# Kernel tuning notes

Hardware: AMD Instinct MI355X
Metric: run time of the kernel (lower is better)

The kernel has to match this reference:

```python
import jax, jax.numpy as jnp
import numpy as np

E = 2048        # embedding_dim
H = 16          # num_q_heads
G = 4           # group_size
HKV = H // G    # num_kv_heads = 4
D = E // H      # q_head_dim = 128
KVD = E // G    # kv_head_dim = 512
B, N = 2, 2048


def setup_inputs() -> dict:
    key = jax.random.key(0)
    ks = jax.random.split(key, 5)
    s = 0.02
    return {
        "x": jax.random.normal(ks[0], (B, N, E), jnp.float32),
        "Wq": jax.random.normal(ks[1], (E, E), jnp.float32) * s,
        "Wk": jax.random.normal(ks[2], (KVD, E), jnp.float32) * s,
        "Wv": jax.random.normal(ks[3], (KVD, E), jnp.float32) * s,
        "Wo": jax.random.normal(ks[4], (E, E), jnp.float32) * s,
    }


def reference(x, Wq, Wk, Wv, Wo):
    b, n, _ = x.shape
    # projections (nn.Linear: y = x @ W.T)
    q = x @ Wq.T                              # (b, n, E)
    k = x @ Wk.T                              # (b, n, KVD)
    v = x @ Wv.T                              # (b, n, KVD)
    # split heads: q -> b h n d with h=H, then (h g) -> g,h layout
    q = q.reshape(b, n, H, D).transpose(0, 2, 1, 3)          # b H n d
    q = q.reshape(b, HKV, G, n, D).transpose(0, 2, 1, 3, 4)  # b g h n d  (h=HKV)
    k = k.reshape(b, n, HKV, D).transpose(0, 2, 1, 3)        # b h s d
    v = v.reshape(b, n, HKV, D).transpose(0, 2, 1, 3)        # b h s d
    scale = 1.0 / jnp.sqrt(jnp.asarray(D, x.dtype))
    scores = jnp.einsum('bghnd,bhsd->bghns', q, k) * scale   # full score tensor
    scores = jax.nn.softmax(scores, axis=-1)
    # dropout p=0.0 -> identity
    o = jnp.einsum('bghns,bhsd->bghnd', scores, v)           # b g h n d
    # rearrange 'b g h n d -> b n (h g) d' then concat heads
    o = o.transpose(0, 3, 2, 1, 4).reshape(b, n, E)          # b n (h g) d -> b n E
    return o @ Wo.T
```

## Files before the change

kernel.cpp:

```cpp
#include <hip/hip_runtime.h>
#include <hip/hip_bf16.h>
#include <cstdint>
#include <cstddef>

using u16 = unsigned short;
typedef __bf16 bf16x8 __attribute__((ext_vector_type(8)));
typedef float f32x4 __attribute__((ext_vector_type(4)));
typedef float f32x16 __attribute__((ext_vector_type(16)));
typedef u16 u16x4 __attribute__((ext_vector_type(4)));
typedef u16 u16x8 __attribute__((ext_vector_type(8)));
typedef uint32_t u32x4 __attribute__((ext_vector_type(4)));

__device__ __forceinline__ u16 f2bf(float f) {
  uint32_t u = __builtin_bit_cast(uint32_t, f);
  u += 0x7FFFu + ((u >> 16) & 1u);
  return (u16)(u >> 16);
}

__device__ __forceinline__ void gld_lds16(const void* g, void* l) {
  __builtin_amdgcn_global_load_lds(
      (const __attribute__((address_space(1))) unsigned int*)g,
      (__attribute__((address_space(3))) unsigned int*)l, 16, 0, 0);
}

#define MFMA16(a, b, c) __builtin_amdgcn_mfma_f32_16x16x32_bf16((a), (b), (c), 0, 0, 0)
#define MFMA32(a, b, c) __builtin_amdgcn_mfma_f32_32x32x16_bf16((a), (b), (c), 0, 0, 0)

__device__ __forceinline__ uint32_t pkbf(float a, float b) {
  uint32_t d;
  asm("v_cvt_pk_bf16_f32 %0, %1, %2" : "=v"(d) : "v"(a), "v"(b));
  return d;
}
__device__ __forceinline__ void swap32(uint32_t& a, uint32_t& b) {
  asm volatile("v_permlane32_swap_b32 %0, %1" : "+v"(a), "+v"(b));
}

__global__ void cvt_kernel(const float* __restrict__ in, u16* __restrict__ out, int n4) {
  int i = blockIdx.x * blockDim.x + threadIdx.x;
  int stride = gridDim.x * blockDim.x;
  for (; i < n4; i += stride) {
    float4 v = reinterpret_cast<const float4*>(in)[i];
    u16x4 o;
    o[0] = f2bf(v.x); o[1] = f2bf(v.y); o[2] = f2bf(v.z); o[3] = f2bf(v.w);
    reinterpret_cast<u16x4*>(out)[i] = o;
  }
}

__global__ void cvt4_kernel(const float* __restrict__ x, const float* __restrict__ Wq,
                            const float* __restrict__ Wk, const float* __restrict__ Wv,
                            u16* __restrict__ xb, u16* __restrict__ Wc) {
  int i = blockIdx.x * blockDim.x + threadIdx.x;
  int stride = gridDim.x * blockDim.x;
  for (; i < 3670016; i += stride) {
    const float* src; u16* dst; int off;
    if (i < 2097152)      { src = x;  dst = xb;            off = i; }
    else if (i < 3145728) { src = Wq; dst = Wc;            off = i - 2097152; }
    else if (i < 3407872) { src = Wk; dst = Wc + 4194304;  off = i - 3145728; }
    else                  { src = Wv; dst = Wc + 5242880;  off = i - 3407872; }
    float4 v = reinterpret_cast<const float4*>(src)[off];
    u16x4 o;
    o[0] = f2bf(v.x); o[1] = f2bf(v.y); o[2] = f2bf(v.z); o[3] = f2bf(v.w);
    reinterpret_cast<u16x4*>(dst)[off] = o;
  }
}

template <bool OUT_BF16>
__global__ __launch_bounds__(256) void gemm_bt(const u16* __restrict__ A,
                                               const u16* __restrict__ B,
                                               void* __restrict__ Cv,
                                               int M, int N, int K) {
  __shared__ __align__(16) u16 Ash[3][128 * 32];
  __shared__ __align__(16) u16 Bsh[3][128 * 32];
  const int tid = threadIdx.x;
  const int w = tid >> 6, lane = tid & 63, ql = lane & 15, g = lane >> 4;
  const int wr = w >> 1, wc = w & 1;
  const int bid = blockIdx.y * gridDim.x + blockIdx.x;
  const int nwg = gridDim.x * gridDim.y;
  const int wg = (bid & 7) * (nwg >> 3) + (bid >> 3);
  const int m0 = (wg / gridDim.x) * 128, n0 = (wg % gridDim.x) * 128;
  const int srow = w * 16 + (lane >> 2);
  const int sk = (lane & 3) * 8;
  const u16* Abase = A + (size_t)(m0 + srow) * K + sk;
  const u16* Bbase = B + (size_t)(n0 + srow) * K + sk;

  f32x4 acc[4][4];
#pragma unroll
  for (int i = 0; i < 4; i++)
#pragma unroll
    for (int j = 0; j < 4; j++) acc[i][j] = f32x4{0.f, 0.f, 0.f, 0.f};

  auto stage = [&](int bi, int tile) {
    const int kt = tile * 32;
    gld_lds16(Abase + kt,                  &Ash[bi][w * 512]);
    gld_lds16(Abase + (size_t)64 * K + kt, &Ash[bi][2048 + w * 512]);
    gld_lds16(Bbase + kt,                  &Bsh[bi][w * 512]);
    gld_lds16(Bbase + (size_t)64 * K + kt, &Bsh[bi][2048 + w * 512]);
  };

  const int nt = K >> 5;
  stage(0, 0);
  stage(1, 1);
  asm volatile("s_waitcnt vmcnt(4)" ::: "memory");
  __builtin_amdgcn_sched_barrier(0);
  __builtin_amdgcn_s_barrier();
  __builtin_amdgcn_sched_barrier(0);

  int cur = 0;
  for (int t = 0; t < nt; ++t) {
    if (t + 2 < nt) {
      int stg = cur + 2; if (stg >= 3) stg -= 3;
      stage(stg, t + 2);
    }
    bf16x8 af[4], bfr[4];
#pragma unroll
    for (int i = 0; i < 4; i++)
      af[i] = *reinterpret_cast<const bf16x8*>(&Ash[cur][(wr * 64 + i * 16 + ql) * 32 + g * 8]);
#pragma unroll
    for (int j = 0; j < 4; j++)
      bfr[j] = *reinterpret_cast<const bf16x8*>(&Bsh[cur][(wc * 64 + j * 16 + ql) * 32 + g * 8]);
    __builtin_amdgcn_s_setprio(1);
#pragma unroll
    for (int i = 0; i < 4; i++)
#pragma unroll
      for (int j = 0; j < 4; j++)
        acc[i][j] = MFMA16(af[i], bfr[j], acc[i][j]);
    __builtin_amdgcn_s_setprio(0);
    if (t + 1 < nt) {
      if (t + 2 < nt) {
        asm volatile("s_waitcnt vmcnt(4)" ::: "memory");
      } else {
        asm volatile("s_waitcnt vmcnt(0)" ::: "memory");
      }
      __builtin_amdgcn_sched_barrier(0);
      __builtin_amdgcn_s_barrier();
      __builtin_amdgcn_sched_barrier(0);
    }
    cur = (cur == 2) ? 0 : cur + 1;
  }

#pragma unroll
  for (int i = 0; i < 4; i++)
#pragma unroll
    for (int j = 0; j < 4; j++)
#pragma unroll
      for (int r = 0; r < 4; r++) {
        const int row = m0 + wr * 64 + i * 16 + g * 4 + r;
        const int col = n0 + wc * 64 + j * 16 + ql;
        if constexpr (OUT_BF16)
          ((u16*)Cv)[(size_t)row * N + col] = f2bf(acc[i][j][r]);
        else
          ((float*)Cv)[(size_t)row * N + col] = acc[i][j][r];
      }
}

__global__ __launch_bounds__(256, 2) void attn_kernel(const u16* __restrict__ QKV,
                                                      u16* __restrict__ O) {
  __shared__ __align__(16) u16 Kb[2][64 * 128];
  __shared__ __align__(16) u16 Vb[3][2][128 * 32];
  const int tid = threadIdx.x, w = tid >> 6, lane = tid & 63;
  const int lq = lane & 31, hi = lane >> 5;
  const int bid = blockIdx.x;
  const int swz = (bid & 7) * 64 + (bid >> 3);
  const int qt = swz & 15;
  const int bh = swz >> 4;
  const int b = bh >> 4, h = bh & 15, hkv = h >> 2;
  const size_t rowb = (size_t)b * 2048;
  const int qbase = qt * 128 + w * 32;

  const u16* Kg = QKV + 2048 + hkv * 128;
  const u16* Vg = QKV + 2560 + hkv * 128;

  bf16x8 bq[8];
  {
    const u16* qp = QKV + (rowb + qbase + lq) * 3072 + h * 128 + hi * 8;
#pragma unroll
    for (int s5 = 0; s5 < 8; s5++)
      bq[s5] = *reinterpret_cast<const bf16x8*>(qp + s5 * 16);
  }

  const int dg = tid & 7, sl = tid >> 3;

  f32x16 oacc[4], lacc;
#pragma unroll
  for (int dt = 0; dt < 4; dt++)
#pragma unroll
    for (int i = 0; i < 16; i++) oacc[dt][i] = 0.f;
#pragma unroll
  for (int i = 0; i < 16; i++) lacc[i] = 0.f;
  float m = -INFINITY;
  const float CEXP = 0.08838834764831845f * 1.4426950408889634f;

  const bf16x8 ones = __builtin_bit_cast(bf16x8,
      u32x4{0x3F803F80u, 0x3F803F80u, 0x3F803F80u, 0x3F803F80u});

  auto stageK = [&](int pb2, int sbase) {
#pragma unroll
    for (int p = 0; p < 4; p++) {
      const int L = p * 2048 + tid * 8;
      const int s = L >> 7;
      const int gI = (L >> 3) & 15;
      gld_lds16(Kg + (rowb + sbase + s) * 3072 + ((gI ^ (s & 7)) << 3),
                &Kb[pb2][p * 2048 + w * 512]);
    }
  };
  auto writeV = [&](int vb3, const u16x8& a00, const u16x8& a01,
                    const u16x8& a10, const u16x8& a11) {
#pragma unroll
    for (int sh2 = 0; sh2 < 2; sh2++)
#pragma unroll
      for (int hf = 0; hf < 2; hf++) {
        const u16x8 v = sh2 ? (hf ? a11 : a10) : (hf ? a01 : a00);
#pragma unroll
        for (int j = 0; j < 8; j++) {
          const int d = dg * 16 + hf * 8 + j;
          const int key = ((d >> 1) ^ (d >> 4)) & 3;
          Vb[vb3][sh2][d * 32 + (sl ^ (key << 3))] = v[j];
        }
      }
  };

#define KFRAG(PB, SH, S5) \
  (*reinterpret_cast<const bf16x8*>(&Kb[PB][((SH)*32 + lq) * 128 + ((((S5)*2 + hi) ^ (lq & 7)) << 3)]))
#define VFRAG(VB, DT, SS) \
  (*reinterpret_cast<const bf16x8*>(&Vb[VB][(SS) >> 1][((DT)*32 + lq) * 32 + \
      ((((SS) & 1) * 16 + hi * 8) ^ (((((DT)*32 + lq) >> 1) ^ (((DT)*32 + lq) >> 4)) & 3) << 3)]))

  u16x8 v00, v01, v10, v11;
  {
    const u16* vp = Vg + (rowb + sl) * 3072 + dg * 16;
    v00 = *reinterpret_cast<const u16x8*>(vp);
    v01 = *reinterpret_cast<const u16x8*>(vp + 8);
    const u16* vp2 = vp + (size_t)32 * 3072;
    v10 = *reinterpret_cast<const u16x8*>(vp2);
    v11 = *reinterpret_cast<const u16x8*>(vp2 + 8);
  }
  stageK(0, 0);
  writeV(0, v00, v01, v10, v11);
  __syncthreads();

  bf16x8 pf0, pf1, pf2, pf3;
  int vprev = 2, vcur = 0, vnext = 1;

#pragma unroll 1
  for (int sb = 0; sb < 32; sb++) {
    const int pb = sb & 1;
    if (sb < 31) {
      const u16* vp = Vg + (rowb + (sb + 1) * 64 + sl) * 3072 + dg * 16;
      v00 = *reinterpret_cast<const u16x8*>(vp);
      v01 = *reinterpret_cast<const u16x8*>(vp + 8);
      const u16* vp2 = vp + (size_t)32 * 3072;
      v10 = *reinterpret_cast<const u16x8*>(vp2);
      v11 = *reinterpret_cast<const u16x8*>(vp2 + 8);
      stageK(pb ^ 1, (sb + 1) * 64);
    }

    f32x16 sc0, sc1;
#pragma unroll
    for (int i = 0; i < 16; i++) { sc0[i] = 0.f; sc1[i] = 0.f; }
    __builtin_amdgcn_s_setprio(1);
#pragma unroll
    for (int s5 = 0; s5 < 8; s5++) {
      sc0 = MFMA32(KFRAG(pb, 0, s5), bq[s5], sc0);
      sc1 = MFMA32(KFRAG(pb, 1, s5), bq[s5], sc1);
    }
    __builtin_amdgcn_s_setprio(0);

    if (sb) {
      __builtin_amdgcn_s_setprio(1);
#pragma unroll
      for (int dt = 0; dt < 4; dt++) {
        oacc[dt] = MFMA32(VFRAG(vprev, dt, 0), pf0, oacc[dt]);
        oacc[dt] = MFMA32(VFRAG(vprev, dt, 1), pf1, oacc[dt]);
        oacc[dt] = MFMA32(VFRAG(vprev, dt, 2), pf2, oacc[dt]);
        oacc[dt] = MFMA32(VFRAG(vprev, dt, 3), pf3, oacc[dt]);
      }
      __builtin_amdgcn_s_setprio(0);
    }

    float u[16];
#pragma unroll
    for (int i = 0; i < 16; i++) u[i] = fmaxf(sc0[i], sc1[i]);
#pragma unroll
    for (int i = 0; i < 8; i++) u[i] = fmaxf(u[i], u[i + 8]);
#pragma unroll
    for (int i = 0; i < 4; i++) u[i] = fmaxf(u[i], u[i + 4]);
    float mx = fmaxf(fmaxf(u[0], u[1]), fmaxf(u[2], u[3]));
    mx = fmaxf(mx, __shfl_xor(mx, 32));

    if (__any((mx - m) * CEXP > 8.0f)) {
      const float mn = fmaxf(m, mx);
      const float corr = exp2f((m - mn) * CEXP);
#pragma unroll
      for (int i = 0; i < 16; i++) lacc[i] *= corr;
#pragma unroll
      for (int dt = 0; dt < 4; dt++)
#pragma unroll
        for (int i = 0; i < 16; i++) oacc[dt][i] *= corr;
      m = mn;
    }

    const float mC = m * CEXP;
    float e0[16], e1[16];
#pragma unroll
    for (int i = 0; i < 16; i++) {
      e0[i] = exp2f(fmaf(sc0[i], CEXP, -mC));
      e1[i] = exp2f(fmaf(sc1[i], CEXP, -mC));
    }
    {
      uint32_t a, bw;
      u32x4 f;
      a = pkbf(e0[0], e0[1]);  bw = pkbf(e0[4], e0[5]);  swap32(a, bw);
      f[0] = a; f[2] = bw;
      a = pkbf(e0[2], e0[3]);  bw = pkbf(e0[6], e0[7]);  swap32(a, bw);
      f[1] = a; f[3] = bw;
      pf0 = __builtin_bit_cast(bf16x8, f);
      a = pkbf(e0[8], e0[9]);  bw = pkbf(e0[12], e0[13]); swap32(a, bw);
      f[0] = a; f[2] = bw;
      a = pkbf(e0[10], e0[11]); bw = pkbf(e0[14], e0[15]); swap32(a, bw);
      f[1] = a; f[3] = bw;
      pf1 = __builtin_bit_cast(bf16x8, f);
      a = pkbf(e1[0], e1[1]);  bw = pkbf(e1[4], e1[5]);  swap32(a, bw);
      f[0] = a; f[2] = bw;
      a = pkbf(e1[2], e1[3]);  bw = pkbf(e1[6], e1[7]);  swap32(a, bw);
      f[1] = a; f[3] = bw;
      pf2 = __builtin_bit_cast(bf16x8, f);
      a = pkbf(e1[8], e1[9]);  bw = pkbf(e1[12], e1[13]); swap32(a, bw);
      f[0] = a; f[2] = bw;
      a = pkbf(e1[10], e1[11]); bw = pkbf(e1[14], e1[15]); swap32(a, bw);
      f[1] = a; f[3] = bw;
      pf3 = __builtin_bit_cast(bf16x8, f);
    }

    lacc = MFMA32(ones, pf0, lacc);
    lacc = MFMA32(ones, pf1, lacc);
    lacc = MFMA32(ones, pf2, lacc);
    lacc = MFMA32(ones, pf3, lacc);

    if (sb < 31) writeV(vnext, v00, v01, v10, v11);
    __syncthreads();

    const int tmp = vprev; vprev = vcur; vcur = vnext; vnext = tmp;
  }

  {
    __builtin_amdgcn_s_setprio(1);
#pragma unroll
    for (int dt = 0; dt < 4; dt++) {
      oacc[dt] = MFMA32(VFRAG(vprev, dt, 0), pf0, oacc[dt]);
      oacc[dt] = MFMA32(VFRAG(vprev, dt, 1), pf1, oacc[dt]);
      oacc[dt] = MFMA32(VFRAG(vprev, dt, 2), pf2, oacc[dt]);
      oacc[dt] = MFMA32(VFRAG(vprev, dt, 3), pf3, oacc[dt]);
    }
    __builtin_amdgcn_s_setprio(0);
  }
  __syncthreads();

  const float rl = 1.0f / lacc[0];
  u16* ob = (w < 2) ? &Kb[w][0] : &Vb[w - 2][0][0];
#pragma unroll
  for (int dt = 0; dt < 4; dt++)
#pragma unroll
    for (int rq = 0; rq < 4; rq++) {
      u16x4 pv;
#pragma unroll
      for (int k = 0; k < 4; k++) pv[k] = f2bf(oacc[dt][rq * 4 + k] * rl);
      *reinterpret_cast<u16x4*>(&ob[lq * 136 + dt * 32 + rq * 8 + hi * 4]) = pv;
    }
  const int orow = lane >> 1, och = (lane & 1) * 64;
  u16* og = O + (rowb + qbase + orow) * 2048 + h * 128 + och;
#pragma unroll
  for (int t = 0; t < 8; t++) {
    u16x8 v = *reinterpret_cast<const u16x8*>(&ob[orow * 136 + och + t * 8]);
    *reinterpret_cast<u16x8*>(og + t * 8) = v;
  }
#undef KFRAG
#undef VFRAG
}

extern "C" void kernel_launch(void* const* d_in, const int* in_sizes, int n_in,
                              void* d_out, int out_size, void* d_ws, size_t ws_size,
                              hipStream_t stream) {
  (void)in_sizes; (void)n_in; (void)out_size;
  const float* x  = (const float*)d_in[0];
  const float* Wq = (const float*)d_in[1];
  const float* Wk = (const float*)d_in[2];
  const float* Wv = (const float*)d_in[3];
  const float* Wo = (const float*)d_in[4];

  if (ws_size < (size_t)(8388608 + 6291456 + 12582912) * 2) return;
  u16* xb  = (u16*)d_ws;
  u16* Wc  = xb + 8388608;
  u16* QKV = Wc + 6291456;
  u16* Ob  = xb;

  cvt4_kernel<<<2048, 256, 0, stream>>>(x, Wq, Wk, Wv, xb, Wc);
  gemm_bt<true><<<dim3(24, 32), 256, 0, stream>>>(xb, Wc, (void*)QKV, 4096, 3072, 2048);
  cvt_kernel<<<2048, 256, 0, stream>>>(Wo, Wc, 1048576);
  attn_kernel<<<dim3(512), 256, 0, stream>>>(QKV, Ob);
  gemm_bt<false><<<dim3(16, 32), 256, 0, stream>>>(Ob, Wc, d_out, 4096, 2048, 2048);
}
```

Measured before the change: 232.5 us.

## Stage V via direct global-to-LDS loads and read with transposing LDS loads

Replaces the register round-trip that scattered V element-by-element into a swizzled transposed LDS layout with direct global_load_lds staging of V, double-buffered like K. PV products now read V fragments through ds_read_b64_tr_b16 transposed loads and swap MFMA operand roles, so the output accumulator becomes transposed and the final normalization goes through an LDS row-sum buffer. This removes many scalar LDS stores and VGPR pressure from V staging. In exchange, the PV step is no longer deferred by one iteration to overlap with the next QK step, and each cluster waits on lgkmcnt(0), which may serialize LDS reads with MFMA.

Result: no change. 229.7 us (-1.2%).

```diff
diff --git a/kernel.cpp b/kernel.cpp
--- a/kernel.cpp
+++ b/kernel.cpp
@@ -9,6 +9,7 @@
 typedef float f32x16 __attribute__((ext_vector_type(16)));
 typedef u16 u16x4 __attribute__((ext_vector_type(4)));
 typedef u16 u16x8 __attribute__((ext_vector_type(8)));
+typedef uint32_t u32x2 __attribute__((ext_vector_type(2)));
 typedef uint32_t u32x4 __attribute__((ext_vector_type(4)));
 
 __device__ __forceinline__ u16 f2bf(float f) {
@@ -33,6 +34,9 @@
 }
 __device__ __forceinline__ void swap32(uint32_t& a, uint32_t& b) {
   asm volatile("v_permlane32_swap_b32 %0, %1" : "+v"(a), "+v"(b));
+}
+__device__ __forceinline__ bf16x8 mk8(u32x2 a, u32x2 b) {
+  return __builtin_bit_cast(bf16x8, u32x4{a[0], a[1], b[0], b[1]});
 }
 
 __global__ void cvt_kernel(const float* __restrict__ in, u16* __restrict__ out, int n4) {
@@ -153,10 +157,29 @@
       }
 }
 
+#define TRRD(D, B, IMM) \
+  asm volatile("ds_read_b64_tr_b16 %0, %1 offset:" #IMM : "=v"(D) : "v"(B))
+
+#define PV_CLUSTER(PF, O0, O1, O2, O3, O4, O5, O6, O7)                          \
+  do {                                                                          \
+    u32x2 a0, a1, b0, b1, c0, c1, d0, d1;                                       \
+    TRRD(a0, ab, O0); TRRD(a1, ab, O1); TRRD(b0, ab, O2); TRRD(b1, ab, O3);     \
+    TRRD(c0, ab, O4); TRRD(c1, ab, O5); TRRD(d0, ab, O6); TRRD(d1, ab, O7);     \
+    asm volatile("s_waitcnt lgkmcnt(0)" ::: "memory");                          \
+    __builtin_amdgcn_sched_barrier(0);                                          \
+    __builtin_amdgcn_s_setprio(1);                                              \
+    oacc[0] = MFMA32(PF, mk8(a0, a1), oacc[0]);                                 \
+    oacc[1] = MFMA32(PF, mk8(b0, b1), oacc[1]);                                 \
+    oacc[2] = MFMA32(PF, mk8(c0, c1), oacc[2]);                                 \
+    oacc[3] = MFMA32(PF, mk8(d0, d1), oacc[3]);                                 \
+    __builtin_amdgcn_s_setprio(0);                                              \
+  } while (0)
+
 __global__ __launch_bounds__(256, 2) void attn_kernel(const u16* __restrict__ QKV,
                                                       u16* __restrict__ O) {
-  __shared__ __align__(16) u16 Kb[2][64 * 128];
-  __shared__ __align__(16) u16 Vb[3][2][128 * 32];
+  __shared__ __align__(16) u16 SHK[2 * 8192];
+  __shared__ __align__(16) u16 SHV[2 * 8320];
+  __shared__ float lbuf[4][32];
   const int tid = threadIdx.x, w = tid >> 6, lane = tid & 63;
   const int lq = lane & 31, hi = lane >> 5;
   const int bid = blockIdx.x;
@@ -178,8 +201,6 @@
       bq[s5] = *reinterpret_cast<const bf16x8*>(qp + s5 * 16);
   }
 
-  const int dg = tid & 7, sl = tid >> 3;
-
   f32x16 oacc[4], lacc;
 #pragma unroll
   for (int dt = 0; dt < 4; dt++)
@@ -200,58 +221,39 @@
       const int s = L >> 7;
       const int gI = (L >> 3) & 15;
       gld_lds16(Kg + (rowb + sbase + s) * 3072 + ((gI ^ (s & 7)) << 3),
-                &Kb[pb2][p * 2048 + w * 512]);
+                &SHK[pb2 * 8192 + p * 2048 + w * 512]);
     }
   };
-  auto writeV = [&](int vb3, const u16x8& a00, const u16x8& a01,
-                    const u16x8& a10, const u16x8& a11) {
-#pragma unroll
-    for (int sh2 = 0; sh2 < 2; sh2++)
-#pragma unroll
-      for (int hf = 0; hf < 2; hf++) {
-        const u16x8 v = sh2 ? (hf ? a11 : a10) : (hf ? a01 : a00);
-#pragma unroll
-        for (int j = 0; j < 8; j++) {
-          const int d = dg * 16 + hf * 8 + j;
-          const int key = ((d >> 1) ^ (d >> 4)) & 3;
-          Vb[vb3][sh2][d * 32 + (sl ^ (key << 3))] = v[j];
-        }
-      }
+  auto stageV = [&](int pb2, int sbase) {
+#pragma unroll
+    for (int c = 0; c < 4; c++) {
+      const int idx = w * 4 + c;
+      const int dg = idx >> 1, half = idx & 1;
+      const int s = half * 32 + (lane >> 1);
+      const int dr0 = (lane & 1) * 8;
+      gld_lds16(Vg + (rowb + sbase + s) * 3072 + dg * 16 + dr0,
+                &SHV[pb2 * 8320 + dg * 1040 + half * 512]);
+    }
   };
 
 #define KFRAG(PB, SH, S5) \
-  (*reinterpret_cast<const bf16x8*>(&Kb[PB][((SH)*32 + lq) * 128 + ((((S5)*2 + hi) ^ (lq & 7)) << 3)]))
-#define VFRAG(VB, DT, SS) \
-  (*reinterpret_cast<const bf16x8*>(&Vb[VB][(SS) >> 1][((DT)*32 + lq) * 32 + \
-      ((((SS) & 1) * 16 + hi * 8) ^ (((((DT)*32 + lq) >> 1) ^ (((DT)*32 + lq) >> 4)) & 3) << 3)]))
-
-  u16x8 v00, v01, v10, v11;
-  {
-    const u16* vp = Vg + (rowb + sl) * 3072 + dg * 16;
-    v00 = *reinterpret_cast<const u16x8*>(vp);
-    v01 = *reinterpret_cast<const u16x8*>(vp + 8);
-    const u16* vp2 = vp + (size_t)32 * 3072;
-    v10 = *reinterpret_cast<const u16x8*>(vp2);
-    v11 = *reinterpret_cast<const u16x8*>(vp2 + 8);
-  }
+  (*reinterpret_cast<const bf16x8*>(&SHK[(PB)*8192 + ((SH)*32 + lq) * 128 + ((((S5)*2 + hi) ^ (lq & 7)) << 3)]))
+
+  const uint32_t vbase0 =
+      (uint32_t)(uintptr_t)(__attribute__((address_space(3))) u16*)&SHV[0];
+  const uint32_t vlane = vbase0 + ((lane >> 4) & 1) * 2080u + (lane >> 5) * 256u
+                       + (lane & 15) * 8u;
+
   stageK(0, 0);
-  writeV(0, v00, v01, v10, v11);
+  stageV(0, 0);
   __syncthreads();
-
-  bf16x8 pf0, pf1, pf2, pf3;
-  int vprev = 2, vcur = 0, vnext = 1;
 
 #pragma unroll 1
   for (int sb = 0; sb < 32; sb++) {
     const int pb = sb & 1;
     if (sb < 31) {
-      const u16* vp = Vg + (rowb + (sb + 1) * 64 + sl) * 3072 + dg * 16;
-      v00 = *reinterpret_cast<const u16x8*>(vp);
-      v01 = *reinterpret_cast<const u16x8*>(vp + 8);
-      const u16* vp2 = vp + (size_t)32 * 3072;
-      v10 = *reinterpret_cast<const u16x8*>(vp2);
-      v11 = *reinterpret_cast<const u16x8*>(vp2 + 8);
       stageK(pb ^ 1, (sb + 1) * 64);
+      stageV(pb ^ 1, (sb + 1) * 64);
     }
 
     f32x16 sc0, sc1;
@@ -265,18 +267,6 @@
     }
     __builtin_amdgcn_s_setprio(0);
 
-    if (sb) {
-      __builtin_amdgcn_s_setprio(1);
-#pragma unroll
-      for (int dt = 0; dt < 4; dt++) {
-        oacc[dt] = MFMA32(VFRAG(vprev, dt, 0), pf0, oacc[dt]);
-        oacc[dt] = MFMA32(VFRAG(vprev, dt, 1), pf1, oacc[dt]);
-        oacc[dt] = MFMA32(VFRAG(vprev, dt, 2), pf2, oacc[dt]);
-        oacc[dt] = MFMA32(VFRAG(vprev, dt, 3), pf3, oacc[dt]);
-      }
-      __builtin_amdgcn_s_setprio(0);
-    }
-
     float u[16];
 #pragma unroll
     for (int i = 0; i < 16; i++) u[i] = fmaxf(sc0[i], sc1[i]);
@@ -306,6 +296,7 @@
       e0[i] = exp2f(fmaf(sc0[i], CEXP, -mC));
       e1[i] = exp2f(fmaf(sc1[i], CEXP, -mC));
     }
+    bf16x8 pf0, pf1, pf2, pf3;
     {
       uint32_t a, bw;
       u32x4 f;
@@ -336,35 +327,26 @@
     lacc = MFMA32(ones, pf2, lacc);
     lacc = MFMA32(ones, pf3, lacc);
 
-    if (sb < 31) writeV(vnext, v00, v01, v10, v11);
+    {
+      const uint32_t ab = vlane + (uint32_t)(pb * 16640);
+      PV_CLUSTER(pf0, 0, 128, 4160, 4288, 8320, 8448, 12480, 12608);
+      PV_CLUSTER(pf1, 512, 640, 4672, 4800, 8832, 8960, 12992, 13120);
+      PV_CLUSTER(pf2, 1024, 1152, 5184, 5312, 9344, 9472, 13504, 13632);
+      PV_CLUSTER(pf3, 1536, 1664, 5696, 5824, 9856, 9984, 14016, 14144);
+    }
+
     __syncthreads();
-
-    const int tmp = vprev; vprev = vcur; vcur = vnext; vnext = tmp;
-  }
-
-  {
-    __builtin_amdgcn_s_setprio(1);
-#pragma unroll
-    for (int dt = 0; dt < 4; dt++) {
-      oacc[dt] = MFMA32(VFRAG(vprev, dt, 0), pf0, oacc[dt]);
-      oacc[dt] = MFMA32(VFRAG(vprev, dt, 1), pf1, oacc[dt]);
-      oacc[dt] = MFMA32(VFRAG(vprev, dt, 2), pf2, oacc[dt]);
-      oacc[dt] = MFMA32(VFRAG(vprev, dt, 3), pf3, oacc[dt]);
-    }
-    __builtin_amdgcn_s_setprio(0);
-  }
+  }
+
+  if (hi == 0) lbuf[w][lq] = lacc[0];
   __syncthreads();
-
-  const float rl = 1.0f / lacc[0];
-  u16* ob = (w < 2) ? &Kb[w][0] : &Vb[w - 2][0][0];
+  u16* ob = (w < 2) ? &SHK[w * 8192] : &SHV[(w - 2) * 8320];
 #pragma unroll
   for (int dt = 0; dt < 4; dt++)
 #pragma unroll
-    for (int rq = 0; rq < 4; rq++) {
-      u16x4 pv;
-#pragma unroll
-      for (int k = 0; k < 4; k++) pv[k] = f2bf(oacc[dt][rq * 4 + k] * rl);
-      *reinterpret_cast<u16x4*>(&ob[lq * 136 + dt * 32 + rq * 8 + hi * 4]) = pv;
+    for (int r = 0; r < 16; r++) {
+      const int qr = (r & 3) + 8 * (r >> 2) + 4 * hi;
+      ob[qr * 136 + dt * 32 + lq] = f2bf(oacc[dt][r] * (1.0f / lbuf[w][qr]));
     }
   const int orow = lane >> 1, och = (lane & 1) * 64;
   u16* og = O + (rowb + qbase + orow) * 2048 + h * 128 + och;
@@ -374,7 +356,6 @@
     *reinterpret_cast<u16x8*>(og + t * 8) = v;
   }
 #undef KFRAG
-#undef VFRAG
 }
 
 extern "C" void kernel_launch(void* const* d_in, const int* in_sizes, int n_in,
```
